# Optimization experiments

Hardware: AMD Instinct MI355X
Metric: run time of the kernel (lower is better)

Reference implementation:

```python
import jax, jax.numpy as jnp
import numpy as np

EMB = 512
HEADS = 8
B, T = 8, 1024

def setup_inputs() -> dict:
    key = jax.random.key(0)
    ks = jax.random.split(key, 6)
    e, h = EMB, HEADS
    s = 1.0 / np.sqrt(e)
    x = jax.random.normal(ks[0], (B, T, e), dtype=jnp.float32)
    # Linear(emb, emb*heads, bias=False): stored as (e, e*h) for x @ W
    Wk = jax.random.normal(ks[1], (e, e * h), dtype=jnp.float32) * s
    Wq = jax.random.normal(ks[2], (e, e * h), dtype=jnp.float32) * s
    Wv = jax.random.normal(ks[3], (e, e * h), dtype=jnp.float32) * s
    # unifyheads: Linear(heads*emb, emb) with bias
    Wu = jax.random.normal(ks[4], (e * h, e), dtype=jnp.float32) * (1.0 / np.sqrt(e * h))
    bu = jax.random.normal(ks[5], (e,), dtype=jnp.float32) * 0.01
    return {"x": x, "Wk": Wk, "Wq": Wq, "Wv": Wv, "Wu": Wu, "bu": bu}

def reference(x, Wk, Wq, Wv, Wu, bu):
    b, t, e = x.shape
    h = HEADS
    scale = e ** (-0.25)  # applied to both q and k, as in the torch code
    q = (x @ Wq).reshape(b, t, h, e) * scale  # (b,t,h,e)
    k = (x @ Wk).reshape(b, t, h, e) * scale
    v = (x @ Wv).reshape(b, t, h, e)
    dot = jnp.einsum('bqhe,bkhe->bhqk', q, k)      # (b,h,t,t)
    attn = jax.nn.softmax(dot, axis=-1)
    out = jnp.einsum('bhqk,bkhe->bqhe', attn, v)    # (b,t,h,e)
    out = out.reshape(b, t, h * e)
    return out @ Wu + bu                            # (b,t,e)
```

## Files before the change

kernel.cpp:

```cpp
#include <hip/hip_runtime.h>
#include <hip/hip_bf16.h>
#include <cstdint>

typedef __attribute__((ext_vector_type(8))) short bf16x8;
typedef __attribute__((ext_vector_type(4))) float f32x4;

typedef __attribute__((address_space(1))) const void gv_t;
typedef __attribute__((address_space(3))) void lv_t;

__device__ __forceinline__ unsigned short f2b(float f) {
  __hip_bfloat16 h = __float2bfloat16(f);
  return __builtin_bit_cast(unsigned short, h);
}
__device__ __forceinline__ float b2f(unsigned short u) {
  unsigned int x = (unsigned int)u << 16;
  return __builtin_bit_cast(float, x);
}

__global__ __launch_bounds__(256) void k_cast(const float* __restrict__ src,
                                              unsigned short* __restrict__ dst, int n4) {
  int i = blockIdx.x * 256 + threadIdx.x;
  if (i >= n4) return;
  const float4 v = ((const float4*)src)[i];
  ushort4 o;
  o.x = f2b(v.x); o.y = f2b(v.y); o.z = f2b(v.z); o.w = f2b(v.w);
  ((ushort4*)dst)[i] = o;
}

__global__ void k_transpose_cast(const float* __restrict__ src,
                                 unsigned short* __restrict__ dst, int R, int C) {
  __shared__ float tile[32][33];
  const int tx = threadIdx.x, ty = threadIdx.y;
  const int c0 = blockIdx.x * 32, r0 = blockIdx.y * 32;
#pragma unroll
  for (int i = 0; i < 32; i += 8)
    tile[ty + i][tx] = src[(long)(r0 + ty + i) * C + (c0 + tx)];
  __syncthreads();
#pragma unroll
  for (int i = 0; i < 32; i += 8)
    dst[(long)(c0 + ty + i) * R + (r0 + tx)] = f2b(tile[tx][ty + i]);
}

__global__ void k_transpose_cast3(const float* __restrict__ s0, const float* __restrict__ s1,
                                  const float* __restrict__ s2,
                                  unsigned short* __restrict__ dst, int R, int C) {
  const float* src = (blockIdx.z == 0) ? s0 : ((blockIdx.z == 1) ? s1 : s2);
  unsigned short* d = dst + (size_t)blockIdx.z * R * C;
  __shared__ float tile[32][33];
  const int tx = threadIdx.x, ty = threadIdx.y;
  const int c0 = blockIdx.x * 32, r0 = blockIdx.y * 32;
#pragma unroll
  for (int i = 0; i < 32; i += 8)
    tile[ty + i][tx] = src[(long)(r0 + ty + i) * C + (c0 + tx)];
  __syncthreads();
#pragma unroll
  for (int i = 0; i < 32; i += 8)
    d[(long)(c0 + ty + i) * R + (r0 + tx)] = f2b(tile[tx][ty + i]);
}

__global__ __launch_bounds__(256) void k_rowsum(const unsigned short* __restrict__ E,
                                                float* __restrict__ rs) {
  const long row = blockIdx.x;
  const unsigned short* p = E + row * 1024;
  const int tid = threadIdx.x;
  const ushort4 raw = ((const ushort4*)p)[tid];
  float s = (b2f(raw.x) + b2f(raw.y)) + (b2f(raw.z) + b2f(raw.w));
#pragma unroll
  for (int off = 32; off >= 1; off >>= 1) s += __shfl_xor(s, off, 64);
  __shared__ float red[4];
  if ((tid & 63) == 0) red[tid >> 6] = s;
  __syncthreads();
  if (tid == 0) rs[row] = (red[0] + red[1]) + (red[2] + red[3]);
}

enum { EPI_QK = 0, EPI_VT = 1, EPI_S = 2, EPI_PV = 3, EPI_OUT = 4 };

template <int EPI>
__global__ __launch_bounds__(256)
void k_gemm(const unsigned short* __restrict__ A, const unsigned short* __restrict__ Bt,
            void* __restrict__ Cv, int K, int lda, int ldb,
            long sA, long sB, float scale, const float* __restrict__ aux) {
  const int z = blockIdx.z;
  A += (long)z * sA;
  Bt += (long)z * sB;
  const int m0 = blockIdx.y * 128;
  const int n0 = blockIdx.x * 128;
  __shared__ __align__(16) unsigned short As[2][128 * 32];
  __shared__ __align__(16) unsigned short Bs[2][128 * 32];
  const int tid = threadIdx.x;
  const int lane = tid & 63;
  const int wm = ((tid >> 6) >> 1) * 64;
  const int wn = ((tid >> 6) & 1) * 64;
  const int srow = tid >> 2;
  const int scol = (tid & 3) * 8;
  f32x4 acc[4][4] = {};

  const unsigned short* ga = A + (long)(m0 + srow) * lda + scol;
  const unsigned short* gb = Bt + (long)(n0 + srow) * ldb + scol;

#define STAGE(buf, koff) do {                                                                        \
    __builtin_amdgcn_global_load_lds((gv_t*)(ga + (koff)), (lv_t*)(&As[buf][tid * 8]), 16, 0, 0);     \
    __builtin_amdgcn_global_load_lds((gv_t*)(ga + 64L * lda + (koff)), (lv_t*)(&As[buf][tid * 8 + 2048]), 16, 0, 0); \
    __builtin_amdgcn_global_load_lds((gv_t*)(gb + (koff)), (lv_t*)(&Bs[buf][tid * 8]), 16, 0, 0);     \
    __builtin_amdgcn_global_load_lds((gv_t*)(gb + 64L * ldb + (koff)), (lv_t*)(&Bs[buf][tid * 8 + 2048]), 16, 0, 0); \
  } while (0)

  STAGE(0, 0);
  for (int k0 = 0; k0 < K; k0 += 32) {
    const int cur = (k0 >> 5) & 1;
    __syncthreads();
    if (k0 + 32 < K) { STAGE(cur ^ 1, k0 + 32); }
    const unsigned short* ap = &As[cur][(wm + (lane & 15)) * 32 + (lane >> 4) * 8];
    const unsigned short* bp = &Bs[cur][(wn + (lane & 15)) * 32 + (lane >> 4) * 8];
    bf16x8 fa[4], fb[4];
#pragma unroll
    for (int i = 0; i < 4; ++i) fa[i] = *(const bf16x8*)(ap + i * 16 * 32);
#pragma unroll
    for (int i = 0; i < 4; ++i) fb[i] = *(const bf16x8*)(bp + i * 16 * 32);
#pragma unroll
    for (int mi = 0; mi < 4; ++mi)
#pragma unroll
      for (int ni = 0; ni < 4; ++ni)
        acc[mi][ni] = __builtin_amdgcn_mfma_f32_16x16x32_bf16(fa[mi], fb[ni], acc[mi][ni], 0, 0, 0);
  }
#undef STAGE

#pragma unroll
  for (int mi = 0; mi < 4; ++mi) {
#pragma unroll
    for (int ni = 0; ni < 4; ++ni) {
#pragma unroll
      for (int r = 0; r < 4; ++r) {
        const int row = m0 + wm + mi * 16 + ((lane >> 4) * 4 + r);
        const int col = n0 + wn + ni * 16 + (lane & 15);
        const float v = acc[mi][ni][r];
        if (EPI == EPI_QK) {
          unsigned short* o = (unsigned short*)Cv;
          const int sec = col >> 12;
          const int cc = col & 4095;
          const long addr = (long)sec * 33554432 +
              ((long)((row >> 10) * 8 + (cc >> 9)) * 1024 + (row & 1023)) * 512 + (cc & 511);
          o[addr] = f2b(v * scale);
        } else if (EPI == EPI_VT) {
          unsigned short* o = (unsigned short*)Cv;
          const long addr = (long)((col >> 10) * 8 + (row >> 9)) * 524288 +
                            (long)(row & 511) * 1024 + (col & 1023);
          o[addr] = f2b(v);
        } else if (EPI == EPI_S) {
          unsigned short* o = (unsigned short*)Cv;
          o[(long)z * 1048576 + (long)row * 1024 + col] = f2b(__expf(v));
        } else if (EPI == EPI_PV) {
          unsigned short* o = (unsigned short*)Cv;
          const float val = v / aux[(long)z * 1024 + row];
          const long addr = (long)(z >> 3) * 4194304 + (long)row * 4096 + (long)(z & 7) * 512 + col;
          o[addr] = f2b(val);
        } else {
          float* o = (float*)Cv;
          o[(long)row * 512 + col] = v + aux[col];
        }
      }
    }
  }
}

extern "C" void kernel_launch(void* const* d_in, const int* in_sizes, int n_in,
                              void* d_out, int out_size, void* d_ws, size_t ws_size,
                              hipStream_t stream) {
  const float* x  = (const float*)d_in[0];
  const float* Wk = (const float*)d_in[1];
  const float* Wq = (const float*)d_in[2];
  const float* Wv = (const float*)d_in[3];
  const float* Wu = (const float*)d_in[4];
  const float* bu = (const float*)d_in[5];
  float* out = (float*)d_out;
  char* ws = (char*)d_ws;

  const size_t NEED1 = 243302400;
  const size_t NEED2 = 260112384;
  const size_t NEED4 = 293732352;
  if (ws_size < NEED1) return;
  const int CH = (ws_size >= NEED4) ? 4 : ((ws_size >= NEED2) ? 2 : 1);

  unsigned short* wut   = (unsigned short*)(ws + 0);
  unsigned short* wtqkv = (unsigned short*)(ws + 4194304);
  unsigned short* xb    = (unsigned short*)(ws + 16777216);
  unsigned short* qb    = (unsigned short*)(ws + 25165824);
  unsigned short* kb    = qb + 33554432;
  unsigned short* vtb   = qb + 67108864;
  unsigned short* Sbuf  = (unsigned short*)(ws + 226492416);
  float*          rs    = (float*)(Sbuf + (size_t)CH * 8388608);

  const float s4 = 0.21022410381342865f;

  k_cast<<<4096, 256, 0, stream>>>(x, xb, 1048576);
  k_transpose_cast3<<<dim3(128, 16, 3), dim3(32, 8), 0, stream>>>(Wq, Wk, Wv, wtqkv, 512, 4096);
  k_transpose_cast<<<dim3(16, 128), dim3(32, 8), 0, stream>>>(Wu, wut, 4096, 512);

  k_gemm<EPI_QK><<<dim3(64, 64, 1), 256, 0, stream>>>(xb, wtqkv, qb, 512, 512, 512, 0, 0, s4, nullptr);
  k_gemm<EPI_VT><<<dim3(64, 32, 1), 256, 0, stream>>>(wtqkv + 4194304, xb, vtb, 512, 512, 512, 0, 0, 1.0f, nullptr);

  for (int b = 0; b < 8; b += CH) {
    const long aoff = (long)b * 4194304;
    k_gemm<EPI_S><<<dim3(8, 8, CH * 8), 256, 0, stream>>>(qb + aoff, kb + aoff, Sbuf,
                                                          512, 512, 512, 524288, 524288, 1.0f, nullptr);
    k_rowsum<<<CH * 8192, 256, 0, stream>>>(Sbuf, rs);
    k_gemm<EPI_PV><<<dim3(4, 8, CH * 8), 256, 0, stream>>>(Sbuf, vtb + aoff, qb + aoff,
                                                           1024, 1024, 1024, 1048576, 524288, 1.0f, rs);
  }

  k_gemm<EPI_OUT><<<dim3(4, 64, 1), 256, 0, stream>>>(qb, wut, out, 4096, 4096, 4096, 0, 0, 1.0f, bu);
}
```

Before: 542.2 us.

## Add 256x256 tiled 8-wave GEMM with swizzled LDS for QKV projections

```diff
diff --git a/kernel.cpp b/kernel.cpp
--- a/kernel.cpp
+++ b/kernel.cpp
@@ -74,6 +74,138 @@
 }
 
 enum { EPI_QK = 0, EPI_VT = 1, EPI_S = 2, EPI_PV = 3, EPI_OUT = 4 };
+
+
+#define BAR256() do { asm volatile("" ::: "memory"); __builtin_amdgcn_s_barrier(); asm volatile("" ::: "memory"); } while (0)
+#define WAITVM(n) do { asm volatile("s_waitcnt vmcnt(" #n ")" ::: "memory"); __builtin_amdgcn_sched_barrier(0); } while (0)
+
+#define STAGE_A(tt, hw, qq)                                                                     \
+  __builtin_amdgcn_global_load_lds(                                                            \
+    (gv_t*)(A + (long)(m0 + (hw)*128 + (qq)*64 + rr) * lda + ((tt) << 6) + csw),               \
+    (lv_t*)(&L[(((((tt)&1)*2 + (hw))*128 + (qq)*64 + rr))*64 + c0]), 16, 0, 0)
+
+#define STAGE_B(tt, qi)                                                                         \
+  __builtin_amdgcn_global_load_lds(                                                            \
+    (gv_t*)(Bt + (long)(n0 + (qi)*64 + rr) * ldb + ((tt) << 6) + csw),                         \
+    (lv_t*)(&L[32768 + (((((tt)&1)*2 + ((qi)>>1))*128 + ((qi)&1)*64 + rr))*64 + c0]), 16, 0, 0)
+
+#define PHASE(slot, QR, QC) do {                                                                \
+    const unsigned short* Abase = &L[((slot)*2 + wr) * 8192];                                   \
+    const unsigned short* Bbase = &L[32768 + ((slot)*2 + (wc>>1)) * 8192];                      \
+    bf16x8 afr[4][2], bfr[2][2];                                                                \
+    _Pragma("unroll")                                                                           \
+    for (int fr = 0; fr < 4; ++fr) {                                                            \
+      const int rA = (QR)*64 + fr*16 + l15;                                                     \
+      _Pragma("unroll")                                                                         \
+      for (int kk = 0; kk < 2; ++kk) {                                                          \
+        const int cA = (kk*32 + l4*8) ^ ((rA & 7) << 3);                                        \
+        afr[fr][kk] = *(const bf16x8*)(Abase + rA*64 + cA);                                     \
+      }                                                                                         \
+    }                                                                                           \
+    _Pragma("unroll")                                                                           \
+    for (int fc = 0; fc < 2; ++fc) {                                                            \
+      const int rB = (wc&1)*64 + (QC)*32 + fc*16 + l15;                                         \
+      _Pragma("unroll")                                                                         \
+      for (int kk = 0; kk < 2; ++kk) {                                                          \
+        const int cB = (kk*32 + l4*8) ^ ((rB & 7) << 3);                                        \
+        bfr[fc][kk] = *(const bf16x8*)(Bbase + rB*64 + cB);                                     \
+      }                                                                                         \
+    }                                                                                           \
+    __builtin_amdgcn_s_setprio(1);                                                              \
+    _Pragma("unroll")                                                                           \
+    for (int fr = 0; fr < 4; ++fr)                                                              \
+      _Pragma("unroll")                                                                         \
+      for (int fc = 0; fc < 2; ++fc)                                                            \
+        _Pragma("unroll")                                                                       \
+        for (int kk = 0; kk < 2; ++kk)                                                          \
+          acc[(QR)*4+fr][(QC)*2+fc] = __builtin_amdgcn_mfma_f32_16x16x32_bf16(                  \
+              afr[fr][kk], bfr[fc][kk], acc[(QR)*4+fr][(QC)*2+fc], 0, 0, 0);                    \
+    __builtin_amdgcn_s_setprio(0);                                                              \
+  } while (0)
+
+template <int EPI>
+__global__ __launch_bounds__(512)
+void k_gemm256(const unsigned short* __restrict__ A, const unsigned short* __restrict__ Bt,
+               void* __restrict__ Cv, int K, int lda, int ldb,
+               long sA, long sB, float scale, const float* __restrict__ aux) {
+  const int z = blockIdx.z;
+  A += (long)z * sA;
+  Bt += (long)z * sB;
+  const int m0 = blockIdx.y * 256;
+  const int n0 = blockIdx.x * 256;
+  __shared__ __align__(16) unsigned short L[65536];
+  const int tid = threadIdx.x;
+  const int lane = tid & 63;
+  const int wid = tid >> 6;
+  const int wr = wid >> 2;
+  const int wc = wid & 3;
+  const int l15 = lane & 15;
+  const int l4 = lane >> 4;
+  const int rr = tid >> 3;
+  const int c0 = (tid & 7) * 8;
+  const int csw = c0 ^ ((rr & 7) << 3);
+
+  f32x4 acc[8][4] = {};
+  const int NT = K >> 6;
+
+  STAGE_A(0, 0, 0); STAGE_A(0, 1, 0); STAGE_A(0, 0, 1); STAGE_A(0, 1, 1);
+  STAGE_B(0, 0); STAGE_B(0, 1); STAGE_B(0, 2); STAGE_B(0, 3);
+  if (NT > 1) {
+    STAGE_A(1, 0, 0); STAGE_A(1, 1, 0);
+    WAITVM(2);
+  } else {
+    WAITVM(0);
+  }
+  __builtin_amdgcn_s_barrier();
+  asm volatile("" ::: "memory");
+
+  for (int t = 0; t < NT; ++t) {
+    const int slot = t & 1;
+    if (t + 1 < NT) { STAGE_A(t + 1, 0, 1); STAGE_A(t + 1, 1, 1); }
+    PHASE(slot, 0, 0);
+    BAR256();
+    if (t + 1 < NT) { STAGE_B(t + 1, 0); STAGE_B(t + 1, 1); }
+    PHASE(slot, 0, 1);
+    BAR256();
+    if (t + 1 < NT) { STAGE_B(t + 1, 2); STAGE_B(t + 1, 3); }
+    if (t + 2 < NT) { STAGE_A(t + 2, 0, 0); STAGE_A(t + 2, 1, 0); }
+    PHASE(slot, 1, 0);
+    BAR256();
+    PHASE(slot, 1, 1);
+    if (t + 1 < NT) {
+      if (t + 2 < NT) WAITVM(2);
+      else            WAITVM(0);
+      __builtin_amdgcn_s_barrier();
+      asm volatile("" ::: "memory");
+    }
+  }
+
+#pragma unroll
+  for (int i = 0; i < 8; ++i) {
+#pragma unroll
+    for (int j = 0; j < 4; ++j) {
+#pragma unroll
+      for (int r = 0; r < 4; ++r) {
+        const int row = m0 + wr * 128 + i * 16 + l4 * 4 + r;
+        const int col = n0 + wc * 64 + j * 16 + l15;
+        const float v = acc[i][j][r];
+        if (EPI == EPI_QK) {
+          unsigned short* o = (unsigned short*)Cv;
+          const int sec = col >> 12;
+          const int cc = col & 4095;
+          const long addr = (long)sec * 33554432 +
+              ((long)((row >> 10) * 8 + (cc >> 9)) * 1024 + (row & 1023)) * 512 + (cc & 511);
+          o[addr] = f2b(v * scale);
+        } else if (EPI == EPI_VT) {
+          unsigned short* o = (unsigned short*)Cv;
+          const long addr = (long)((col >> 10) * 8 + (row >> 9)) * 524288 +
+                            (long)(row & 511) * 1024 + (col & 1023);
+          o[addr] = f2b(v);
+        }
+      }
+    }
+  }
+}
 
 template <int EPI>
 __global__ __launch_bounds__(256)
@@ -134,19 +266,7 @@
         const int row = m0 + wm + mi * 16 + ((lane >> 4) * 4 + r);
         const int col = n0 + wn + ni * 16 + (lane & 15);
         const float v = acc[mi][ni][r];
-        if (EPI == EPI_QK) {
-          unsigned short* o = (unsigned short*)Cv;
-          const int sec = col >> 12;
-          const int cc = col & 4095;
-          const long addr = (long)sec * 33554432 +
-              ((long)((row >> 10) * 8 + (cc >> 9)) * 1024 + (row & 1023)) * 512 + (cc & 511);
-          o[addr] = f2b(v * scale);
-        } else if (EPI == EPI_VT) {
-          unsigned short* o = (unsigned short*)Cv;
-          const long addr = (long)((col >> 10) * 8 + (row >> 9)) * 524288 +
-                            (long)(row & 511) * 1024 + (col & 1023);
-          o[addr] = f2b(v);
-        } else if (EPI == EPI_S) {
+        if (EPI == EPI_S) {
           unsigned short* o = (unsigned short*)Cv;
           o[(long)z * 1048576 + (long)row * 1024 + col] = f2b(__expf(v));
         } else if (EPI == EPI_PV) {
@@ -196,8 +316,8 @@
   k_transpose_cast3<<<dim3(128, 16, 3), dim3(32, 8), 0, stream>>>(Wq, Wk, Wv, wtqkv, 512, 4096);
   k_transpose_cast<<<dim3(16, 128), dim3(32, 8), 0, stream>>>(Wu, wut, 4096, 512);
 
-  k_gemm<EPI_QK><<<dim3(64, 64, 1), 256, 0, stream>>>(xb, wtqkv, qb, 512, 512, 512, 0, 0, s4, nullptr);
-  k_gemm<EPI_VT><<<dim3(64, 32, 1), 256, 0, stream>>>(wtqkv + 4194304, xb, vtb, 512, 512, 512, 0, 0, 1.0f, nullptr);
+  k_gemm256<EPI_QK><<<dim3(32, 32, 1), 512, 0, stream>>>(xb, wtqkv, qb, 512, 512, 512, 0, 0, s4, nullptr);
+  k_gemm256<EPI_VT><<<dim3(32, 16, 1), 512, 0, stream>>>(wtqkv + 4194304, xb, vtb, 512, 512, 512, 0, 0, 1.0f, nullptr);
 
   for (int b = 0; b < 8; b += CH) {
     const long aoff = (long)b * 4194304;
```

Measured after the change: 532.8 us. No clear change (-1.7%).
